# Kernel tuning notes

Measured on AMD Instinct MI355X. Metric: run time of the kernel, lower is better.

## Reference

```python
import jax, jax.numpy as jnp
import numpy as np
from jax import lax

B, C_IN, D, H, W = 1, 64, 48, 48, 48
R = 3
PC = 64          # proj_channels
OC = 128         # out_channels
K = (2 * R + 1) ** 3  # 343 offsets
OFFSETS = np.array([(dz, dy, dx)
                    for dz in range(-R, R + 1)
                    for dy in range(-R, R + 1)
                    for dx in range(-R, R + 1)], dtype=np.int32)


def setup_inputs() -> dict:
    key = jax.random.key(0)
    ks = jax.random.split(key, 10)
    s = 0.05
    return {
        'source_features': jax.random.normal(ks[0], (B, C_IN, D, H, W), jnp.float32),
        'warped_target_features': jax.random.normal(ks[1], (B, C_IN, D, H, W), jnp.float32),
        'proj_src_w': jax.random.normal(ks[2], (PC, C_IN, 1, 1, 1), jnp.float32) * s,
        'proj_src_b': jax.random.normal(ks[3], (PC,), jnp.float32) * s,
        'proj_tgt_w': jax.random.normal(ks[4], (PC, C_IN, 1, 1, 1), jnp.float32) * s,
        'proj_tgt_b': jax.random.normal(ks[5], (PC,), jnp.float32) * s,
        'enc1_w': jax.random.normal(ks[6], (OC, K + 3, 3, 3, 3), jnp.float32) * s,
        'enc1_b': jax.random.normal(ks[7], (OC,), jnp.float32) * s,
        'enc2_w': jax.random.normal(ks[8], (OC, OC, 3, 3, 3), jnp.float32) * s,
        'enc2_b': jax.random.normal(ks[9], (OC,), jnp.float32) * s,
    }


def conv3d(x, w, b, pad):
    out = lax.conv_general_dilated(
        x, w, window_strides=(1, 1, 1), padding=[(pad, pad)] * 3,
        dimension_numbers=('NCDHW', 'OIDHW', 'NCDHW'))
    return out + b[None, :, None, None, None]


def l2norm_c(x):
    # torch F.normalize(dim=1): x / max(||x||_2, 1e-12)
    n = jnp.sqrt(jnp.sum(x * x, axis=1, keepdims=True))
    return x / jnp.maximum(n, 1e-12)


def instance_norm(x, eps=1e-5):
    # InstanceNorm3d, affine=False: per (B,C), biased var over D,H,W
    m = jnp.mean(x, axis=(2, 3, 4), keepdims=True)
    v = jnp.var(x, axis=(2, 3, 4), keepdims=True)
    return (x - m) * lax.rsqrt(v + eps)


def reference(source_features, warped_target_features,
              proj_src_w, proj_src_b, proj_tgt_w, proj_tgt_b,
              enc1_w, enc1_b, enc2_w, enc2_b):
    sp = l2norm_c(conv3d(source_features, proj_src_w, proj_src_b, 0))
    tp = l2norm_c(conv3d(warped_target_features, proj_tgt_w, proj_tgt_b, 0))
    padded = jnp.pad(tp, ((0, 0), (0, 0), (R, R), (R, R), (R, R)), mode='edge')
    offs = jnp.asarray(OFFSETS)  # [K,3] int32

    def corr_one(off):
        # shifted window of padded target, dot over channels -> [B,D,H,W]
        shifted = lax.dynamic_slice(
            padded, (0, 0, R + off[0], R + off[1], R + off[2]), sp.shape)
        return jnp.sum(sp * shifted, axis=1)

    corr = lax.map(corr_one, offs)          # [K,B,D,H,W]
    corr = jnp.moveaxis(corr, 0, 1)         # [B,K,D,H,W]

    # online-softmax expected offset == softmax over K weighted by offset vecs
    wts = jax.nn.softmax(corr, axis=1)
    eo = jnp.einsum('bkdhw,kc->bcdhw', wts, offs.astype(sp.dtype))  # [B,3,D,H,W]

    feat = jnp.concatenate([corr, eo], axis=1)  # [B,K+3,D,H,W]
    h = conv3d(feat, enc1_w, enc1_b, 1)
    h = jax.nn.gelu(instance_norm(h), approximate=False)
    h = conv3d(h, enc2_w, enc2_b, 1)
    h = jax.nn.gelu(instance_norm(h), approximate=False)
    return h
```

## Files before the change

kernel.cpp:

```cpp
#include <hip/hip_runtime.h>
#include <math.h>
#include <stdint.h>

#define VOL 110592
#define CINP 64
#define PCH 64

typedef short short8 __attribute__((ext_vector_type(8)));
typedef float floatx4 __attribute__((ext_vector_type(4)));
typedef _Float16 h8 __attribute__((ext_vector_type(8)));
typedef _Float16 h2v __attribute__((ext_vector_type(2)));

__device__ __forceinline__ ushort f2bf(float f) {
    union { float f; uint32_t u; } v; v.f = f;
    uint32_t r = v.u + 0x7FFFu + ((v.u >> 16) & 1u);
    return (ushort)(r >> 16);
}

__device__ __forceinline__ float hdot2(h2v a, h2v b, float c) {
#if __has_builtin(__builtin_amdgcn_fdot2)
    return __builtin_amdgcn_fdot2(a, b, c, false);
#else
    return fmaf((float)a[0], (float)b[0], fmaf((float)a[1], (float)b[1], c));
#endif
}

__global__ __launch_bounds__(256) void proj_l2norm_kernel(
    const float* __restrict__ x,
    const float* __restrict__ w,
    const float* __restrict__ b,
    _Float16* __restrict__ out)
{
    const int v = blockIdx.x * 256 + threadIdx.x;
    float xr[CINP];
    for (int ci = 0; ci < CINP; ci++)
        xr[ci] = x[(size_t)ci * VOL + v];

    float acc[PCH];
    for (int c = 0; c < PCH; c++) {
        float a = b[c];
        #pragma unroll
        for (int ci = 0; ci < CINP; ci++)
            a = fmaf(w[c * CINP + ci], xr[ci], a);
        acc[c] = a;
    }
    float s = 0.f;
    #pragma unroll
    for (int c = 0; c < PCH; c++) s += acc[c] * acc[c];
    const float inv = 1.0f / fmaxf(sqrtf(s), 1e-12f);
    #pragma unroll
    for (int c = 0; c < PCH; c++)
        out[(size_t)v * PCH + c] = (_Float16)(acc[c] * inv);
}

__global__ __launch_bounds__(256) void corr_fused_kernel(
    const _Float16* __restrict__ sp,
    const _Float16* __restrict__ tp,
    ushort* __restrict__ featT)
{
    const int t  = threadIdx.x;
    const int c8 = t & 7;
    const int vg = t >> 3;
    const int v  = blockIdx.x * 32 + vg;
    const int x = v % 48, y = (v / 48) % 48, z = v / 2304;

    __shared__ __align__(16) ushort lds[32 * 360];

    const h8 s = *(const h8*)(sp + (size_t)v * PCH + c8 * 8);

    float ssum = 0.f, e0 = 0.f, e1 = 0.f, e2 = 0.f;
    int k = 0;
    for (int dz = -3; dz <= 3; dz++) {
        const int zb = min(max(z + dz, 0), 47) * 2304;
        const float fdz = (float)dz;
        for (int dy = -3; dy <= 3; dy++) {
            const int rb = zb + min(max(y + dy, 0), 47) * 48;
            const float fdy = (float)dy;
            #pragma unroll
            for (int dx = -3; dx <= 3; dx++) {
                const int xc = min(max(x + dx, 0), 47);
                const h8 tv = *(const h8*)(tp + (size_t)(rb + xc) * PCH + c8 * 8);
                float d0 = hdot2((h2v){s[0], s[1]}, (h2v){tv[0], tv[1]}, 0.f);
                d0 = hdot2((h2v){s[2], s[3]}, (h2v){tv[2], tv[3]}, d0);
                float d1 = hdot2((h2v){s[4], s[5]}, (h2v){tv[4], tv[5]}, 0.f);
                d1 = hdot2((h2v){s[6], s[7]}, (h2v){tv[6], tv[7]}, d1);
                float dot = d0 + d1;
                dot += __shfl_xor(dot, 1);
                dot += __shfl_xor(dot, 2);
                dot += __shfl_xor(dot, 4);
                if (c8 == 0) lds[vg * 360 + k] = f2bf(dot);
                const float e = __expf(dot);
                ssum += e;
                e0 += e * fdz;
                e1 += e * fdy;
                e2 += e * (float)dx;
                k++;
            }
        }
    }

    if (c8 == 0) {
        const float inv = 1.f / ssum;
        lds[vg * 360 + 343] = f2bf(e0 * inv);
        lds[vg * 360 + 344] = f2bf(e1 * inv);
        lds[vg * 360 + 345] = f2bf(e2 * inv);
        #pragma unroll
        for (int j = 346; j < 352; j++) lds[vg * 360 + j] = 0;
    }
    __syncthreads();

    ushort* ob = featT + (size_t)blockIdx.x * 32 * 352;
    #pragma unroll
    for (int j = 0; j < 6; j++) {
        const int idx = t + j * 256;
        if (idx < 1408) {
            const int row = idx / 44, col = (idx % 44) * 8;
            *(int4*)(ob + (size_t)row * 352 + col) = *(const int4*)(&lds[row * 360 + col]);
        }
    }
}

template<int CIN, int CPAD>
__global__ __launch_bounds__(256) void wprep_kernel(
    const float* __restrict__ w, ushort* __restrict__ wTo, float* __restrict__ zp)
{
    if (blockIdx.x == 0 && threadIdx.x < 4) zp[threadIdx.x] = 0.f;
    const int oc = blockIdx.x;
    for (int idx = threadIdx.x; idx < CPAD * 27; idx += 256) {
        const int icp = idx / 27, tap = idx - icp * 27;
        float val = 0.f;
        if (icp < CIN) val = w[((size_t)oc * CIN + icp) * 27 + tap];
        wTo[((size_t)tap * 128 + oc) * CPAD + icp] = f2bf(val);
    }
}

template<int CPAD>
__global__ __launch_bounds__(256, 4) void conv3_mfma_kernel(
    const ushort* __restrict__ xT,
    const ushort* __restrict__ wT,
    const float* __restrict__ bias,
    const ushort* __restrict__ zpad,
    float* __restrict__ out)
{
    const int blk = blockIdx.x;
    const int tx = blk % 3, ty = (blk / 3) % 12, tz = blk / 36;
    const int x0 = tx * 16, y0 = ty * 4, z0 = tz * 2;
    const int t = threadIdx.x;
    const int wave = t >> 6;
    const int lane = t & 63;
    const int l = lane & 15;
    const int q = lane >> 4;
    const int ocw = (wave & 1) * 64;
    const int mzw = wave >> 1;

    __shared__ __align__(16) ushort win[432 * 32];

    int off[7];
    #pragma unroll
    for (int it = 0; it < 7; it++) {
        const int c = wave + it * 4;
        off[it] = -1;
        if (c < 27) {
            const int i = c * 64 + lane;
            const int p = i >> 2, g = i & 3;
            const int wz = p / 108, pr = p - wz * 108;
            const int wy = pr / 18, wx = pr - wy * 18;
            const int gz = z0 + wz - 1, gy = y0 + wy - 1, gx = x0 + wx - 1;
            if ((unsigned)gx < 48u && (unsigned)gy < 48u && (unsigned)gz < 48u)
                off[it] = ((gz * 2304 + gy * 48 + gx) * CPAD + g * 8) * 2;
        }
    }

    floatx4 acc[4][4];
    #pragma unroll
    for (int i = 0; i < 4; i++)
        #pragma unroll
        for (int j = 0; j < 4; j++)
            acc[i][j] = (floatx4){0.f, 0.f, 0.f, 0.f};

    const ushort* wbase = wT + (size_t)(ocw + l) * CPAD + q * 8;
    const int ldsbase = (mzw * 108 + l) * 32 + q * 8;

    const int NCH = CPAD / 32;
    #pragma unroll 1
    for (int ck = 0; ck < NCH; ck++) {
        if (ck) __syncthreads();

        const char* xck = (const char*)xT + (size_t)ck * 64;
        #pragma unroll
        for (int it = 0; it < 7; it++) {
            const int c = wave + it * 4;
            if (c < 27) {
                const ushort* gp = (off[it] >= 0)
                    ? (const ushort*)(xck + off[it])
                    : zpad;
                __builtin_amdgcn_global_load_lds(
                    (const __attribute__((address_space(1))) uint32_t*)gp,
                    (__attribute__((address_space(3))) uint32_t*)(win + c * 512 + lane * 8),
                    16, 0, 0);
            }
        }

        const ushort* wck = wbase + ck * 32;
        short8 A0[4], A1[4];
        A0[0] = *(const short8*)(wck);
        A0[1] = *(const short8*)(wck + 16 * CPAD);
        A0[2] = *(const short8*)(wck + 32 * CPAD);
        A0[3] = *(const short8*)(wck + 48 * CPAD);

        __syncthreads();

#define CONV_BODY(TP, AU, AL)                                              \
        {                                                                  \
            const int tpn_ = (TP) + 1;                                     \
            if (tpn_ < 27) {                                               \
                const ushort* wp_ = wck + (size_t)tpn_ * (128 * CPAD);     \
                AL[0] = *(const short8*)(wp_);                             \
                AL[1] = *(const short8*)(wp_ + 16 * CPAD);                 \
                AL[2] = *(const short8*)(wp_ + 32 * CPAD);                 \
                AL[3] = *(const short8*)(wp_ + 48 * CPAD);                 \
            }                                                              \
            const int dz_ = (TP) / 9;                                      \
            const int dy_ = ((TP) / 3) % 3;                                \
            const int dx_ = (TP) % 3;                                      \
            const int pb_ = ldsbase + (dz_ * 108 + dy_ * 18 + dx_) * 32;   \
            const short8 b0_ = *(const short8*)(&win[pb_ +    0]);         \
            const short8 b1_ = *(const short8*)(&win[pb_ +  576]);         \
            const short8 b2_ = *(const short8*)(&win[pb_ + 1152]);         \
            const short8 b3_ = *(const short8*)(&win[pb_ + 1728]);         \
            acc[0][0] = __builtin_amdgcn_mfma_f32_16x16x32_bf16(AU[0], b0_, acc[0][0], 0, 0, 0); \
            acc[1][0] = __builtin_amdgcn_mfma_f32_16x16x32_bf16(AU[1], b0_, acc[1][0], 0, 0, 0); \
            acc[2][0] = __builtin_amdgcn_mfma_f32_16x16x32_bf16(AU[2], b0_, acc[2][0], 0, 0, 0); \
            acc[3][0] = __builtin_amdgcn_mfma_f32_16x16x32_bf16(AU[3], b0_, acc[3][0], 0, 0, 0); \
            acc[0][1] = __builtin_amdgcn_mfma_f32_16x16x32_bf16(AU[0], b1_, acc[0][1], 0, 0, 0); \
            acc[1][1] = __builtin_amdgcn_mfma_f32_16x16x32_bf16(AU[1], b1_, acc[1][1], 0, 0, 0); \
            acc[2][1] = __builtin_amdgcn_mfma_f32_16x16x32_bf16(AU[2], b1_, acc[2][1], 0, 0, 0); \
            acc[3][1] = __builtin_amdgcn_mfma_f32_16x16x32_bf16(AU[3], b1_, acc[3][1], 0, 0, 0); \
            acc[0][2] = __builtin_amdgcn_mfma_f32_16x16x32_bf16(AU[0], b2_, acc[0][2], 0, 0, 0); \
            acc[1][2] = __builtin_amdgcn_mfma_f32_16x16x32_bf16(AU[1], b2_, acc[1][2], 0, 0, 0); \
            acc[2][2] = __builtin_amdgcn_mfma_f32_16x16x32_bf16(AU[2], b2_, acc[2][2], 0, 0, 0); \
            acc[3][2] = __builtin_amdgcn_mfma_f32_16x16x32_bf16(AU[3], b2_, acc[3][2], 0, 0, 0); \
            acc[0][3] = __builtin_amdgcn_mfma_f32_16x16x32_bf16(AU[0], b3_, acc[0][3], 0, 0, 0); \
            acc[1][3] = __builtin_amdgcn_mfma_f32_16x16x32_bf16(AU[1], b3_, acc[1][3], 0, 0, 0); \
            acc[2][3] = __builtin_amdgcn_mfma_f32_16x16x32_bf16(AU[2], b3_, acc[2][3], 0, 0, 0); \
            acc[3][3] = __builtin_amdgcn_mfma_f32_16x16x32_bf16(AU[3], b3_, acc[3][3], 0, 0, 0); \
        }

        #pragma unroll 1
        for (int tg = 0; tg < 13; tg++) {
            const int tp = tg * 2;
            CONV_BODY(tp, A0, A1);
            CONV_BODY(tp + 1, A1, A0);
        }
        CONV_BODY(26, A0, A1);
#undef CONV_BODY
    }

    #pragma unroll
    for (int nt = 0; nt < 4; nt++) {
        const int ocb = ocw + nt * 16 + q * 4;
        const float4 bv = *(const float4*)(bias + ocb);
        #pragma unroll
        for (int mt = 0; mt < 4; mt++) {
            const int v = (z0 + mzw) * 2304 + (y0 + mt) * 48 + x0 + l;
            out[(size_t)(ocb + 0) * VOL + v] = acc[nt][mt][0] + bv.x;
            out[(size_t)(ocb + 1) * VOL + v] = acc[nt][mt][1] + bv.y;
            out[(size_t)(ocb + 2) * VOL + v] = acc[nt][mt][2] + bv.z;
            out[(size_t)(ocb + 3) * VOL + v] = acc[nt][mt][3] + bv.w;
        }
    }
}

__global__ __launch_bounds__(256) void chan_stats_part_kernel(
    const float* __restrict__ x, float* __restrict__ pstats )
{
    const int c = blockIdx.x, g = blockIdx.y;
    const float4* p = (const float4*)(x + (size_t)c * VOL) + g * 3456;
    float s = 0.f, s2 = 0.f;
    #pragma unroll
    for (int j = 0; j < 14; j++) {
        const int i = threadIdx.x + j * 256;
        if (i < 3456) {
            const float4 v = p[i];
            s += v.x + v.y + v.z + v.w;
            s2 = fmaf(v.x, v.x, fmaf(v.y, v.y, fmaf(v.z, v.z, fmaf(v.w, v.w, s2))));
        }
    }
    s  += __shfl_down(s, 32);  s  += __shfl_down(s, 16);
    s  += __shfl_down(s, 8);   s  += __shfl_down(s, 4);
    s  += __shfl_down(s, 2);   s  += __shfl_down(s, 1);
    s2 += __shfl_down(s2, 32); s2 += __shfl_down(s2, 16);
    s2 += __shfl_down(s2, 8);  s2 += __shfl_down(s2, 4);
    s2 += __shfl_down(s2, 2);  s2 += __shfl_down(s2, 1);
    __shared__ float rs[4], rs2[4];
    if ((threadIdx.x & 63) == 0) {
        rs[threadIdx.x >> 6] = s;
        rs2[threadIdx.x >> 6] = s2;
    }
    __syncthreads();
    if (threadIdx.x == 0) {
        pstats[(c * 8 + g) * 2]     = rs[0] + rs[1] + rs[2] + rs[3];
        pstats[(c * 8 + g) * 2 + 1] = rs2[0] + rs2[1] + rs2[2] + rs2[3];
    }
}

__global__ __launch_bounds__(128) void chan_stats_fin_kernel(
    const float* __restrict__ pstats, float* __restrict__ stats )
{
    const int c = threadIdx.x;
    float s = 0.f, s2 = 0.f;
    #pragma unroll
    for (int g = 0; g < 8; g++) {
        s  += pstats[(c * 8 + g) * 2];
        s2 += pstats[(c * 8 + g) * 2 + 1];
    }
    const float mean = s / (float)VOL;
    const float var  = s2 / (float)VOL - mean * mean;
    stats[c * 2]     = mean;
    stats[c * 2 + 1] = rsqrtf(var + 1e-5f);
}

__device__ __forceinline__ float gelu_exact(float h)
{
    return 0.5f * h * (1.f + erff(h * 0.70710678118654752f));
}

__global__ __launch_bounds__(256) void norm_gelu_kernel(
    const float* __restrict__ x, const float* __restrict__ stats,
    float* __restrict__ out)
{
    const size_t i = (size_t)blockIdx.x * 256 + threadIdx.x;
    const int c = (int)(i / (VOL / 4));
    const float mean = stats[c * 2], rstd = stats[c * 2 + 1];
    const float4 xv = ((const float4*)x)[i];
    float4 o;
    o.x = gelu_exact((xv.x - mean) * rstd);
    o.y = gelu_exact((xv.y - mean) * rstd);
    o.z = gelu_exact((xv.z - mean) * rstd);
    o.w = gelu_exact((xv.w - mean) * rstd);
    ((float4*)out)[i] = o;
}

__global__ __launch_bounds__(256) void norm_gelu_transpose_kernel(
    const float* __restrict__ x, const float* __restrict__ stats,
    ushort* __restrict__ outT)
{
    __shared__ float tile[32][33];
    const int v0 = blockIdx.x * 32;
    const int c0 = blockIdx.y * 32;
    const int t = threadIdx.x;
    const int vl = t & 31, cl = t >> 5;
    #pragma unroll
    for (int i = 0; i < 4; i++) {
        const int c = c0 + cl + i * 8;
        const float mean = stats[c * 2], rstd = stats[c * 2 + 1];
        const float val = x[(size_t)c * VOL + v0 + vl];
        tile[cl + i * 8][vl] = gelu_exact((val - mean) * rstd);
    }
    __syncthreads();
    const int vw = t >> 3, cg = t & 7;
    ushort4 o;
    o.x = f2bf(tile[cg * 4 + 0][vw]);
    o.y = f2bf(tile[cg * 4 + 1][vw]);
    o.z = f2bf(tile[cg * 4 + 2][vw]);
    o.w = f2bf(tile[cg * 4 + 3][vw]);
    *(ushort4*)(outT + (size_t)(v0 + vw) * 128 + c0 + cg * 4) = o;
}

extern "C" void kernel_launch(void* const* d_in, const int* in_sizes, int n_in,
                              void* d_out, int out_size, void* d_ws, size_t ws_size,
                              hipStream_t stream)
{
    const float* src = (const float*)d_in[0];
    const float* tgt = (const float*)d_in[1];
    const float* psw = (const float*)d_in[2];
    const float* psb = (const float*)d_in[3];
    const float* ptw = (const float*)d_in[4];
    const float* ptb = (const float*)d_in[5];
    const float* e1w = (const float*)d_in[6];
    const float* e1b = (const float*)d_in[7];
    const float* e2w = (const float*)d_in[8];
    const float* e2b = (const float*)d_in[9];

    float* ws = (float*)d_ws;
    _Float16* sp  = (_Float16*)ws;
    _Float16* tp  = (_Float16*)(ws + (size_t)32 * VOL);
    ushort* featT = (ushort*)(ws + (size_t)128 * VOL);
    float*  h1    = ws;
    float*  h2    = ws + (size_t)128 * VOL;
    ushort* h1T   = (ushort*)(ws + (size_t)304 * VOL);
    float*  w1Tf  = ws + (size_t)368 * VOL;
    ushort* w1T   = (ushort*)w1Tf;
    float*  w2Tf  = w1Tf + 608256;
    ushort* w2T   = (ushort*)w2Tf;
    float*  stats = w2Tf + 221184;
    float*  pstats = stats + 256;
    float*  zpadf  = pstats + 2048;
    const ushort* zpad = (const ushort*)zpadf;

    wprep_kernel<346, 352><<<128, 256, 0, stream>>>(e1w, w1T, zpadf);
    wprep_kernel<128, 128><<<128, 256, 0, stream>>>(e2w, w2T, zpadf);

    proj_l2norm_kernel<<<432, 256, 0, stream>>>(src, psw, psb, sp);
    proj_l2norm_kernel<<<432, 256, 0, stream>>>(tgt, ptw, ptb, tp);
    corr_fused_kernel<<<3456, 256, 0, stream>>>(sp, tp, featT);

    conv3_mfma_kernel<352><<<864, 256, 0, stream>>>(featT, w1T, e1b, zpad, h1);
    chan_stats_part_kernel<<<dim3(128, 8), 256, 0, stream>>>(h1, pstats);
    chan_stats_fin_kernel<<<1, 128, 0, stream>>>(pstats, stats);
    norm_gelu_transpose_kernel<<<dim3(3456, 4), 256, 0, stream>>>(h1, stats, h1T);

    conv3_mfma_kernel<128><<<864, 256, 0, stream>>>(h1T, w2T, e2b, zpad, h2);
    chan_stats_part_kernel<<<dim3(128, 8), 256, 0, stream>>>(h2, pstats);
    chan_stats_fin_kernel<<<1, 128, 0, stream>>>(pstats, stats);
    norm_gelu_kernel<<<(128 * VOL) / 1024, 256, 0, stream>>>(h2, stats, (float*)d_out);
}
```

Measured before the change: 1.210 ms.

## Load conv B operands directly from global memory instead of LDS window

Drops the shared-memory halo window and its global_load_lds staging and barriers in the 3x3x3 MFMA conv. Each wave now reads its B fragments for every tap straight from global memory, with a zero-pad fallback at the borders. This removes the syncthreads and LDS traffic, but each input voxel is now fetched up to 27 times through the cache, which adds global load latency inside the MFMA loop.

Result: slower. 2.232 ms (+84.5%).

```diff
diff --git a/kernel.cpp b/kernel.cpp
--- a/kernel.cpp
+++ b/kernel.cpp
@@ -153,23 +153,10 @@
     const int ocw = (wave & 1) * 64;
     const int mzw = wave >> 1;
 
-    __shared__ __align__(16) ushort win[432 * 32];
-
-    int off[7];
-    #pragma unroll
-    for (int it = 0; it < 7; it++) {
-        const int c = wave + it * 4;
-        off[it] = -1;
-        if (c < 27) {
-            const int i = c * 64 + lane;
-            const int p = i >> 2, g = i & 3;
-            const int wz = p / 108, pr = p - wz * 108;
-            const int wy = pr / 18, wx = pr - wy * 18;
-            const int gz = z0 + wz - 1, gy = y0 + wy - 1, gx = x0 + wx - 1;
-            if ((unsigned)gx < 48u && (unsigned)gy < 48u && (unsigned)gz < 48u)
-                off[it] = ((gz * 2304 + gy * 48 + gx) * CPAD + g * 8) * 2;
-        }
-    }
+    const int xw = x0 - 1 + l;
+    const int yw = y0 - 1;
+    const int zw = z0 + mzw - 1;
+    const int koff = q * 8;
 
     floatx4 acc[4][4];
     #pragma unroll
@@ -178,37 +165,37 @@
         for (int j = 0; j < 4; j++)
             acc[i][j] = (floatx4){0.f, 0.f, 0.f, 0.f};
 
-    const ushort* wbase = wT + (size_t)(ocw + l) * CPAD + q * 8;
-    const int ldsbase = (mzw * 108 + l) * 32 + q * 8;
+    const ushort* wbase = wT + (size_t)(ocw + l) * CPAD + koff;
 
     const int NCH = CPAD / 32;
     #pragma unroll 1
     for (int ck = 0; ck < NCH; ck++) {
-        if (ck) __syncthreads();
-
-        const char* xck = (const char*)xT + (size_t)ck * 64;
-        #pragma unroll
-        for (int it = 0; it < 7; it++) {
-            const int c = wave + it * 4;
-            if (c < 27) {
-                const ushort* gp = (off[it] >= 0)
-                    ? (const ushort*)(xck + off[it])
-                    : zpad;
-                __builtin_amdgcn_global_load_lds(
-                    (const __attribute__((address_space(1))) uint32_t*)gp,
-                    (__attribute__((address_space(3))) uint32_t*)(win + c * 512 + lane * 8),
-                    16, 0, 0);
-            }
-        }
-
         const ushort* wck = wbase + ck * 32;
+
         short8 A0[4], A1[4];
         A0[0] = *(const short8*)(wck);
         A0[1] = *(const short8*)(wck + 16 * CPAD);
         A0[2] = *(const short8*)(wck + 32 * CPAD);
         A0[3] = *(const short8*)(wck + 48 * CPAD);
 
-        __syncthreads();
+#define BLOAD(BV, TP)                                                      \
+        {                                                                  \
+            const int dz_ = (TP) / 9;                                      \
+            const int dy_ = ((TP) / 3) % 3;                                \
+            const int dx_ = (TP) % 3;                                      \
+            const int zi_ = zw + dz_;                                      \
+            const int gx_ = xw + dx_;                                      \
+            const bool okzx_ = ((unsigned)zi_ < 48u) & ((unsigned)gx_ < 48u);\
+            _Pragma("unroll")                                              \
+            for (int mt_ = 0; mt_ < 4; mt_++) {                            \
+                const int gy_ = yw + mt_ + dy_;                            \
+                const bool ok_ = okzx_ & ((unsigned)gy_ < 48u);            \
+                const int idx_ = (zi_ * 2304 + gy_ * 48 + gx_) * CPAD      \
+                                 + ck * 32 + koff;                         \
+                const ushort* p_ = ok_ ? (xT + idx_) : zpad;               \
+                BV[mt_] = *(const short8*)p_;                              \
+            }                                                              \
+        }
 
 #define CONV_BODY(TP, AU, AL)                                              \
         {                                                                  \
@@ -220,14 +207,12 @@
                 AL[2] = *(const short8*)(wp_ + 32 * CPAD);                 \
                 AL[3] = *(const short8*)(wp_ + 48 * CPAD);                 \
             }                                                              \
-            const int dz_ = (TP) / 9;                                      \
-            const int dy_ = ((TP) / 3) % 3;                                \
-            const int dx_ = (TP) % 3;                                      \
-            const int pb_ = ldsbase + (dz_ * 108 + dy_ * 18 + dx_) * 32;   \
-            const short8 b0_ = *(const short8*)(&win[pb_ +    0]);         \
-            const short8 b1_ = *(const short8*)(&win[pb_ +  576]);         \
-            const short8 b2_ = *(const short8*)(&win[pb_ + 1152]);         \
-            const short8 b3_ = *(const short8*)(&win[pb_ + 1728]);         \
+            short8 B_[4];                                                  \
+            BLOAD(B_, TP)                                                  \
+            const short8 b0_ = B_[0];                                      \
+            const short8 b1_ = B_[1];                                      \
+            const short8 b2_ = B_[2];                                      \
+            const short8 b3_ = B_[3];                                      \
             acc[0][0] = __builtin_amdgcn_mfma_f32_16x16x32_bf16(AU[0], b0_, acc[0][0], 0, 0, 0); \
             acc[1][0] = __builtin_amdgcn_mfma_f32_16x16x32_bf16(AU[1], b0_, acc[1][0], 0, 0, 0); \
             acc[2][0] = __builtin_amdgcn_mfma_f32_16x16x32_bf16(AU[2], b0_, acc[2][0], 0, 0, 0); \
@@ -254,6 +239,7 @@
         }
         CONV_BODY(26, A0, A1);
 #undef CONV_BODY
+#undef BLOAD
     }
 
     #pragma unroll
```
